# Kernel tuning notes

Hardware: AMD Instinct MI355X
Metric: run time of the kernel (lower is better)

Reference implementation:

```python
import jax, jax.numpy as jnp
import numpy as np

EPS = 0.5  # diffusion epsilon from init_kwargs

def setup_inputs() -> dict:
    key = jax.random.key(0)
    k = jax.random.split(key, 7)
    B, N0, N1, n = 1024, 32, 32, 64
    Mu0 = jax.random.normal(k[0], (N0, n), dtype=jnp.float32) * 2.0
    Mu1 = jax.random.normal(k[1], (N1, n), dtype=jnp.float32) * 2.0
    # diagonal covariances must be positive
    S0 = jax.random.uniform(k[2], (N0, n), dtype=jnp.float32, minval=0.1, maxval=1.0)
    S1 = jax.random.uniform(k[3], (N1, n), dtype=jnp.float32, minval=0.1, maxval=1.0)
    Lam = jax.random.uniform(k[4], (N0, N1), dtype=jnp.float32, minval=0.0, maxval=1.0)
    Lam = Lam / Lam.sum()  # transport plan sums to 1
    X = jax.random.normal(k[5], (B, n), dtype=jnp.float32)
    t = jnp.float32(0.3)
    return {"X": X, "Mu0": Mu0, "Mu1": Mu1, "S0": S0, "S1": S1, "Lam": Lam, "t": t}

def reference(X, Mu0, Mu1, S0, S1, Lam, t):
    eps2 = EPS * EPS
    S0e = S0[:, None, :]        # (N0,1,n)
    S1e = S1[None, :, :]        # (1,N1,n)
    Ds = jnp.sqrt(4.0 * S0e * S1e + EPS ** 4)
    Cs = 0.5 * (Ds - eps2)                       # (N0,N1,n)
    mu_t = (1.0 - t) * Mu0[:, None, :] + t * Mu1[None, :, :]  # (N0,N1,n)
    Sigma = (1.0 - t) ** 2 * S0e + t ** 2 * S1e + 2.0 * t * (1.0 - t) * (Cs + 0.5 * eps2)
    # St = Pt - Qt - eps^2 * t
    St = t * S1e + (1.0 - t) * Cs - ((1.0 - t) * S0e + t * Cs) - eps2 * t
    K = St / Sigma                               # (N0,N1,n)
    v = Mu1[None, :, :] - Mu0[:, None, :]        # (N0,N1,n)
    d = X[:, None, None, :] - mu_t               # (B,N0,N1,n)
    U = K * d + v                                # (B,N0,N1,n)
    # diag-Normal log_prob plus n/2*log(2pi) == -0.5*sum(d^2/Sigma + log Sigma)
    logw = -0.5 * jnp.sum(d * d / Sigma + jnp.log(Sigma), axis=-1)  # (B,N0,N1)
    W = jnp.exp(jnp.clip(logw, -50.0, 50.0)) * Lam                  # (B,N0,N1)
    num = jnp.einsum('bijn,bij->bn', U, W)       # (B,n)
    den = jnp.sum(W, axis=(1, 2))[:, None]       # (B,1)
    return num / den
```

## Files before the change

### kernel.cpp

```cpp
#include <hip/hip_runtime.h>
#include <math.h>

#define EPS2f 0.25f
#define EPS4f 0.0625f
#define BB 4

__global__ __launch_bounds__(64) void precomp_kernel(
    const float* __restrict__ Mu0, const float* __restrict__ Mu1,
    const float* __restrict__ S0,  const float* __restrict__ S1,
    const float* __restrict__ tptr,
    float2* __restrict__ AB_T, float2* __restrict__ KV,
    float* __restrict__ C0)
{
    const int ij = blockIdx.x;
    const int k  = threadIdx.x;
    const int i  = ij >> 5;
    const int j  = ij & 31;
    const float t   = *tptr;
    const float omt = 1.0f - t;

    const float s0 = S0[i * 64 + k];
    const float s1 = S1[j * 64 + k];
    const float m0 = Mu0[i * 64 + k];
    const float m1 = Mu1[j * 64 + k];

    const float ds  = sqrtf(4.0f * s0 * s1 + EPS4f);
    const float cs  = 0.5f * (ds - EPS2f);
    const float mt  = omt * m0 + t * m1;
    const float sig = omt * omt * s0 + t * t * s1
                    + 2.0f * t * omt * (cs + 0.5f * EPS2f);
    const float isig = 1.0f / sig;
    const float st = t * s1 - omt * s0 + (omt - t) * cs - EPS2f * t;
    const float kk = st * isig;
    const float v  = m1 - m0;

    AB_T[(k << 10) + ij] = make_float2(isig, 2.0f * mt * isig);
    KV[(ij << 6) + k]    = make_float2(kk, v - kk * mt);

    float c = mt * mt * isig + __logf(sig);
    #pragma unroll
    for (int off = 32; off >= 1; off >>= 1)
        c += __shfl_xor(c, off, 64);
    if (k == 0) C0[ij] = c;
}

__global__ __launch_bounds__(512) void gmm_main_kernel(
    const float* __restrict__ X,   const float* __restrict__ Lam,
    const float* __restrict__ C0,
    const float2* __restrict__ AB_T, const float2* __restrict__ KV,
    float* __restrict__ out)
{
    __shared__ float4 XsT[64];
    __shared__ float4 Wl[1024];
    __shared__ float  denp[8 * BB];
    __shared__ float  red[8 * 64 * BB];

    const int tid  = threadIdx.x;
    const int lane = tid & 63;
    const int w    = tid >> 6;
    const int b0   = blockIdx.x * BB;

    if (tid < 64 * BB) {
        ((float*)XsT)[(tid & 63) * BB + (tid >> 6)] = X[b0 * 64 + tid];
    }
    __syncthreads();

    const int ij0 = tid;
    const int ij1 = tid + 512;
    float q0a = 0.f, q0b = 0.f, q0c = 0.f, q0d = 0.f;
    float q1a = 0.f, q1b = 0.f, q1c = 0.f, q1d = 0.f;
    #pragma unroll 4
    for (int k = 0; k < 64; ++k) {
        const float2 ab0 = AB_T[(k << 10) + ij0];
        const float2 ab1 = AB_T[(k << 10) + ij1];
        const float4 xk  = XsT[k];
        q0a = fmaf(fmaf(ab0.x, xk.x, -ab0.y), xk.x, q0a);
        q0b = fmaf(fmaf(ab0.x, xk.y, -ab0.y), xk.y, q0b);
        q0c = fmaf(fmaf(ab0.x, xk.z, -ab0.y), xk.z, q0c);
        q0d = fmaf(fmaf(ab0.x, xk.w, -ab0.y), xk.w, q0d);
        q1a = fmaf(fmaf(ab1.x, xk.x, -ab1.y), xk.x, q1a);
        q1b = fmaf(fmaf(ab1.x, xk.y, -ab1.y), xk.y, q1b);
        q1c = fmaf(fmaf(ab1.x, xk.z, -ab1.y), xk.z, q1c);
        q1d = fmaf(fmaf(ab1.x, xk.w, -ab1.y), xk.w, q1d);
    }

    const float c00 = C0[ij0], l0 = Lam[ij0];
    const float c01 = C0[ij1], l1 = Lam[ij1];
    #define WCALC(q, c, l) (__expf(fminf(fmaxf(-0.5f * ((q) + (c)), -50.0f), 50.0f)) * (l))
    float4 w0, w1;
    w0.x = WCALC(q0a, c00, l0); w0.y = WCALC(q0b, c00, l0);
    w0.z = WCALC(q0c, c00, l0); w0.w = WCALC(q0d, c00, l0);
    w1.x = WCALC(q1a, c01, l1); w1.y = WCALC(q1b, c01, l1);
    w1.z = WCALC(q1c, c01, l1); w1.w = WCALC(q1d, c01, l1);
    #undef WCALC
    Wl[ij0] = w0;
    Wl[ij1] = w1;

    float d0 = w0.x + w1.x;
    float d1 = w0.y + w1.y;
    float d2 = w0.z + w1.z;
    float d3 = w0.w + w1.w;
    #pragma unroll
    for (int off = 32; off >= 1; off >>= 1) {
        d0 += __shfl_xor(d0, off, 64);
        d1 += __shfl_xor(d1, off, 64);
        d2 += __shfl_xor(d2, off, 64);
        d3 += __shfl_xor(d3, off, 64);
    }
    if (lane == 0) {
        denp[w * BB + 0] = d0;
        denp[w * BB + 1] = d1;
        denp[w * BB + 2] = d2;
        denp[w * BB + 3] = d3;
    }
    __syncthreads();

    const float4 xk4 = XsT[lane];
    float n0 = 0.f, n1 = 0.f, n2 = 0.f, n3 = 0.f;
    const int ijbase = w * 128;
    #pragma unroll 4
    for (int c = 0; c < 128; ++c) {
        const int ij = ijbase + c;
        const float4 wv = Wl[ij];
        const float2 kv = KV[(ij << 6) + lane];
        float u;
        u = fmaf(kv.x, xk4.x, kv.y); n0 = fmaf(wv.x, u, n0);
        u = fmaf(kv.x, xk4.y, kv.y); n1 = fmaf(wv.y, u, n1);
        u = fmaf(kv.x, xk4.z, kv.y); n2 = fmaf(wv.z, u, n2);
        u = fmaf(kv.x, xk4.w, kv.y); n3 = fmaf(wv.w, u, n3);
    }
    {
        float* r = &red[(w * 64 + lane) * BB];
        r[0] = n0; r[1] = n1; r[2] = n2; r[3] = n3;
    }
    __syncthreads();

    if (tid < 256) {
        const int bb = tid >> 6;
        const int k  = tid & 63;
        float s = 0.f, d = 0.f;
        #pragma unroll
        for (int ww = 0; ww < 8; ++ww) {
            s += red[(ww * 64 + k) * BB + bb];
            d += denp[ww * BB + bb];
        }
        out[b0 * 64 + tid] = s / d;
    }
}

extern "C" void kernel_launch(void* const* d_in, const int* in_sizes, int n_in,
                              void* d_out, int out_size, void* d_ws, size_t ws_size,
                              hipStream_t stream) {
    const float* X   = (const float*)d_in[0];
    const float* Mu0 = (const float*)d_in[1];
    const float* Mu1 = (const float*)d_in[2];
    const float* S0  = (const float*)d_in[3];
    const float* S1  = (const float*)d_in[4];
    const float* Lam = (const float*)d_in[5];
    const float* t   = (const float*)d_in[6];
    float* out = (float*)d_out;

    char* ws = (char*)d_ws;
    float2* AB_T = (float2*)(ws);
    float2* KV   = (float2*)(ws + (512 << 10));
    float*  C0   = (float*)(ws + (1024 << 10));

    precomp_kernel<<<1024, 64, 0, stream>>>(Mu0, Mu1, S0, S1, t, AB_T, KV, C0);
    gmm_main_kernel<<<256, 512, 0, stream>>>(X, Lam, C0, AB_T, KV, out);
}
```

Before: 86.84 us.

## Use 1024-thread blocks with one mixture pair per thread and wave-local reduction

The main kernel now launches 1024 threads per block, so each thread handles a single (i,j) pair instead of two. The numerator loop is split so each wave reduces over exactly the 64 pairs whose weights that same wave wrote. This makes the block barrier between the weight write and the numerator pass unnecessary, and it is removed. The reduction scratch buffer gets a stride of 5 to avoid LDS bank conflicts. The aim is twice as many waves per CU for latency hiding and one fewer barrier, at the cost of a larger final cross-wave reduction (16 partials instead of 8).

```diff
diff --git a/kernel.cpp b/kernel.cpp
--- a/kernel.cpp
+++ b/kernel.cpp
@@ -44,7 +44,7 @@
     if (k == 0) C0[ij] = c;
 }
 
-__global__ __launch_bounds__(512) void gmm_main_kernel(
+__global__ __launch_bounds__(1024, 4) void gmm_main_kernel(
     const float* __restrict__ X,   const float* __restrict__ Lam,
     const float* __restrict__ C0,
     const float2* __restrict__ AB_T, const float2* __restrict__ KV,
@@ -52,8 +52,8 @@
 {
     __shared__ float4 XsT[64];
     __shared__ float4 Wl[1024];
-    __shared__ float  denp[8 * BB];
-    __shared__ float  red[8 * 64 * BB];
+    __shared__ float  denp[16 * BB];
+    __shared__ float  red[16 * 64 * 5];
 
     const int tid  = threadIdx.x;
     const int lane = tid & 63;
@@ -65,41 +65,26 @@
     }
     __syncthreads();
 
-    const int ij0 = tid;
-    const int ij1 = tid + 512;
-    float q0a = 0.f, q0b = 0.f, q0c = 0.f, q0d = 0.f;
-    float q1a = 0.f, q1b = 0.f, q1c = 0.f, q1d = 0.f;
-    #pragma unroll 4
+    const int ij = tid;
+    float qa = 0.f, qb = 0.f, qc = 0.f, qd = 0.f;
+    #pragma unroll 8
     for (int k = 0; k < 64; ++k) {
-        const float2 ab0 = AB_T[(k << 10) + ij0];
-        const float2 ab1 = AB_T[(k << 10) + ij1];
-        const float4 xk  = XsT[k];
-        q0a = fmaf(fmaf(ab0.x, xk.x, -ab0.y), xk.x, q0a);
-        q0b = fmaf(fmaf(ab0.x, xk.y, -ab0.y), xk.y, q0b);
-        q0c = fmaf(fmaf(ab0.x, xk.z, -ab0.y), xk.z, q0c);
-        q0d = fmaf(fmaf(ab0.x, xk.w, -ab0.y), xk.w, q0d);
-        q1a = fmaf(fmaf(ab1.x, xk.x, -ab1.y), xk.x, q1a);
-        q1b = fmaf(fmaf(ab1.x, xk.y, -ab1.y), xk.y, q1b);
-        q1c = fmaf(fmaf(ab1.x, xk.z, -ab1.y), xk.z, q1c);
-        q1d = fmaf(fmaf(ab1.x, xk.w, -ab1.y), xk.w, q1d);
+        const float2 ab = AB_T[(k << 10) + ij];
+        const float4 xk = XsT[k];
+        qa = fmaf(fmaf(ab.x, xk.x, -ab.y), xk.x, qa);
+        qb = fmaf(fmaf(ab.x, xk.y, -ab.y), xk.y, qb);
+        qc = fmaf(fmaf(ab.x, xk.z, -ab.y), xk.z, qc);
+        qd = fmaf(fmaf(ab.x, xk.w, -ab.y), xk.w, qd);
     }
 
-    const float c00 = C0[ij0], l0 = Lam[ij0];
-    const float c01 = C0[ij1], l1 = Lam[ij1];
-    #define WCALC(q, c, l) (__expf(fminf(fmaxf(-0.5f * ((q) + (c)), -50.0f), 50.0f)) * (l))
-    float4 w0, w1;
-    w0.x = WCALC(q0a, c00, l0); w0.y = WCALC(q0b, c00, l0);
-    w0.z = WCALC(q0c, c00, l0); w0.w = WCALC(q0d, c00, l0);
-    w1.x = WCALC(q1a, c01, l1); w1.y = WCALC(q1b, c01, l1);
-    w1.z = WCALC(q1c, c01, l1); w1.w = WCALC(q1d, c01, l1);
+    const float c0 = C0[ij], l0 = Lam[ij];
+    #define WCALC(q) (__expf(fminf(fmaxf(-0.5f * ((q) + c0), -50.0f), 50.0f)) * l0)
+    float4 wv4;
+    wv4.x = WCALC(qa); wv4.y = WCALC(qb); wv4.z = WCALC(qc); wv4.w = WCALC(qd);
     #undef WCALC
-    Wl[ij0] = w0;
-    Wl[ij1] = w1;
+    Wl[ij] = wv4;
 
-    float d0 = w0.x + w1.x;
-    float d1 = w0.y + w1.y;
-    float d2 = w0.z + w1.z;
-    float d3 = w0.w + w1.w;
+    float d0 = wv4.x, d1 = wv4.y, d2 = wv4.z, d3 = wv4.w;
     #pragma unroll
     for (int off = 32; off >= 1; off >>= 1) {
         d0 += __shfl_xor(d0, off, 64);
@@ -113,16 +98,15 @@
         denp[w * BB + 2] = d2;
         denp[w * BB + 3] = d3;
     }
-    __syncthreads();
 
     const float4 xk4 = XsT[lane];
     float n0 = 0.f, n1 = 0.f, n2 = 0.f, n3 = 0.f;
-    const int ijbase = w * 128;
-    #pragma unroll 4
-    for (int c = 0; c < 128; ++c) {
-        const int ij = ijbase + c;
-        const float4 wv = Wl[ij];
-        const float2 kv = KV[(ij << 6) + lane];
+    const int ijbase = w * 64;
+    #pragma unroll 8
+    for (int c = 0; c < 64; ++c) {
+        const int ijb = ijbase + c;
+        const float4 wv = Wl[ijb];
+        const float2 kv = KV[(ijb << 6) + lane];
         float u;
         u = fmaf(kv.x, xk4.x, kv.y); n0 = fmaf(wv.x, u, n0);
         u = fmaf(kv.x, xk4.y, kv.y); n1 = fmaf(wv.y, u, n1);
@@ -130,7 +114,7 @@
         u = fmaf(kv.x, xk4.w, kv.y); n3 = fmaf(wv.w, u, n3);
     }
     {
-        float* r = &red[(w * 64 + lane) * BB];
+        float* r = &red[(w * 64 + lane) * 5];
         r[0] = n0; r[1] = n1; r[2] = n2; r[3] = n3;
     }
     __syncthreads();
@@ -140,8 +124,8 @@
         const int k  = tid & 63;
         float s = 0.f, d = 0.f;
         #pragma unroll
-        for (int ww = 0; ww < 8; ++ww) {
-            s += red[(ww * 64 + k) * BB + bb];
+        for (int ww = 0; ww < 16; ++ww) {
+            s += red[(ww * 64 + k) * 5 + bb];
             d += denp[ww * BB + bb];
         }
         out[b0 * 64 + tid] = s / d;
@@ -166,5 +150,5 @@
     float*  C0   = (float*)(ws + (1024 << 10));
 
     precomp_kernel<<<1024, 64, 0, stream>>>(Mu0, Mu1, S0, S1, t, AB_T, KV, C0);
-    gmm_main_kernel<<<256, 512, 0, stream>>>(X, Lam, C0, AB_T, KV, out);
+    gmm_main_kernel<<<256, 1024, 0, stream>>>(X, Lam, C0, AB_T, KV, out);
 }
```

After: 84.80 us. 1.02x faster.
